# Performance work log

Hardware: AMD Instinct MI355X
Metric: run time of the kernel (lower is better)

## Reference

```python
import jax, jax.numpy as jnp
import numpy as np

N = 50000       # nodes
E = 800000      # edges
D = 128         # in_channels == hidden*heads
H = 8           # heads
C = 16          # hidden_channels (per-head dim)
L = 4           # num_layers
OUT = 128       # out_channels


def setup_inputs() -> dict:
    key = jax.random.key(0)
    ks = jax.random.split(key, 16)
    s = 1.0 / np.sqrt(D)
    inp = {
        "x": jax.random.normal(ks[0], (N, D), dtype=jnp.float32),
        "edge_index": jax.random.randint(ks[1], (2, E), 0, N, dtype=jnp.int32),
        "batch": jnp.zeros((N,), dtype=jnp.int32),
        # stacked per-layer params (all layers are D->H*C with D == H*C)
        "Wq": jax.random.normal(ks[2], (L, D, H * C), dtype=jnp.float32) * s,
        "bq": jnp.zeros((L, H * C), dtype=jnp.float32),
        "Wk": jax.random.normal(ks[3], (L, D, H * C), dtype=jnp.float32) * s,
        "bk": jnp.zeros((L, H * C), dtype=jnp.float32),
        "Wv": jax.random.normal(ks[4], (L, D, H * C), dtype=jnp.float32) * s,
        "bv": jnp.zeros((L, H * C), dtype=jnp.float32),
        "Wskip": jax.random.normal(ks[5], (L, D, H * C), dtype=jnp.float32) * s,
        "bskip": jnp.zeros((L, H * C), dtype=jnp.float32),
        "Wout": jax.random.normal(ks[6], (D, OUT), dtype=jnp.float32) * s,
        "bout": jnp.zeros((OUT,), dtype=jnp.float32),
    }
    return inp


def _transformer_conv(x, src, dst, Wq, bq, Wk, bk, Wv, bv, Wskip, bskip):
    # PyG TransformerConv (concat=True, root_weight=True, beta=False), eval mode
    q = (x @ Wq + bq).reshape(N, H, C)
    k = (x @ Wk + bk).reshape(N, H, C)
    v = (x @ Wv + bv).reshape(N, H, C)
    # edge-wise attention scores [E, H]
    score = jnp.einsum("ehc,ehc->eh", q[dst], k[src]) / jnp.sqrt(jnp.float32(C))
    # segment softmax over incoming edges of each dst node
    m = jax.ops.segment_max(score, dst, num_segments=N)          # [N, H]
    p = jnp.exp(score - m[dst])                                  # [E, H]
    z = jax.ops.segment_sum(p, dst, num_segments=N)              # [N, H]
    alpha = p / z[dst]                                           # [E, H]
    msg = alpha[:, :, None] * v[src]                             # [E, H, C]
    agg = jax.ops.segment_sum(msg, dst, num_segments=N)          # [N, H, C]
    return agg.reshape(N, H * C) + (x @ Wskip + bskip)


def reference(x, edge_index, batch, Wq, bq, Wk, bk, Wv, bv, Wskip, bskip, Wout, bout):
    src = edge_index[0]
    dst = edge_index[1]
    for l in range(L):
        x = _transformer_conv(x, src, dst, Wq[l], bq[l], Wk[l], bk[l],
                              Wv[l], bv[l], Wskip[l], bskip[l])
        x = jax.nn.relu(x)  # dropout is identity in eval mode
    return x @ Wout + bout
```

## Files before the change

kernel.cpp:

```cpp
#include <hip/hip_runtime.h>
#include <hip/hip_fp16.h>
#include <math.h>

#define NN 50000
#define EE 800000
#define DD 128

typedef __attribute__((ext_vector_type(8))) _Float16 half8;
typedef __attribute__((ext_vector_type(2))) _Float16 h2;
typedef __attribute__((ext_vector_type(4))) float f32x4;

#if __has_builtin(__builtin_amdgcn_fdot2)
#define FDOT2(a,b,c) __builtin_amdgcn_fdot2((a),(b),(c),false)
#else
static __device__ __forceinline__ float FDOT2(h2 a, h2 b, float c){
  return c + (float)a[0]*(float)b[0] + (float)a[1]*(float)b[1];
}
#endif


__global__ void zero_kernel(int* __restrict__ p, int n){
  int i = blockIdx.x*blockDim.x + threadIdx.x;
  if (i < n) p[i] = 0;
}

__global__ void hist_kernel(const int* __restrict__ edst, int* __restrict__ deg, int e){
  int i = blockIdx.x*blockDim.x + threadIdx.x;
  if (i < e) atomicAdd(&deg[edst[i]], 1);
}

__global__ void scan_partial(const int* __restrict__ deg, int* __restrict__ bsum, int n){
  __shared__ int s[256];
  int t = threadIdx.x;
  int i = blockIdx.x*256 + t;
  s[t] = (i < n) ? deg[i] : 0;
  __syncthreads();
  for (int o = 128; o > 0; o >>= 1){
    if (t < o) s[t] += s[t+o];
    __syncthreads();
  }
  if (t == 0) bsum[blockIdx.x] = s[0];
}

__global__ void scan_bsums(int* __restrict__ bsum, int nb){
  __shared__ int s[256];
  int t = threadIdx.x;
  int v = (t < nb) ? bsum[t] : 0;
  s[t] = v;
  __syncthreads();
  for (int o = 1; o < 256; o <<= 1){
    int x = (t >= o) ? s[t-o] : 0;
    __syncthreads();
    s[t] += x;
    __syncthreads();
  }
  if (t < nb) bsum[t] = s[t] - v;
}

__global__ void scan_apply(const int* __restrict__ deg, const int* __restrict__ bsum,
                           int* __restrict__ off, int* __restrict__ cursor, int n){
  __shared__ int s[256];
  int t = threadIdx.x;
  int i = blockIdx.x*256 + t;
  int v = (i < n) ? deg[i] : 0;
  s[t] = v;
  __syncthreads();
  for (int o = 1; o < 256; o <<= 1){
    int x = (t >= o) ? s[t-o] : 0;
    __syncthreads();
    s[t] += x;
    __syncthreads();
  }
  int excl = s[t] - v + bsum[blockIdx.x];
  if (i < n){
    off[i] = excl;
    if (i < n-1) cursor[i] = excl;
  }
}

__global__ void scatter_kernel(const int* __restrict__ esrc, const int* __restrict__ edst,
                               int* __restrict__ cursor, int* __restrict__ csr_src, int e){
  int i = blockIdx.x*blockDim.x + threadIdx.x;
  if (i < e){
    int d = edst[i];
    int pos = atomicAdd(&cursor[d], 1);
    csr_src[pos] = esrc[i];
  }
}

__global__ void prep_w(const float* __restrict__ Wq, const float* __restrict__ Wk,
                       const float* __restrict__ Wv, const float* __restrict__ Ws,
                       const float* __restrict__ bq, const float* __restrict__ bk,
                       const float* __restrict__ bv, const float* __restrict__ bs,
                       const float* __restrict__ Wout,
                       __half* __restrict__ wt, float* __restrict__ bcat,
                       __half* __restrict__ wtout){
  int idx = blockIdx.x*256 + threadIdx.x;
  if (idx < 4*512*128){
    int l = idx >> 16;
    int rem = idx & 65535;
    int n = rem >> 7;
    int k = rem & 127;
    int mat = n >> 7;
    int nn = n & 127;
    const float* W = (mat==0)?Wq:(mat==1)?Wk:(mat==2)?Wv:Ws;
    wt[idx] = __float2half(W[l*16384 + k*128 + nn]);
  }
  if (idx < 128*128){
    int n = idx >> 7, k = idx & 127;
    wtout[idx] = __float2half(Wout[k*128 + n]);
  }
  if (idx < 4*512){
    int l = idx >> 9, n = idx & 511;
    int mat = n >> 7, nn = n & 127;
    const float* B = (mat==0)?bq:(mat==1)?bk:(mat==2)?bv:bs;
    bcat[idx] = B[l*128 + nn];
  }
}

__global__ void convert_x(const float* __restrict__ x, __half* __restrict__ xh, int n8){
  int i = blockIdx.x*256 + threadIdx.x;
  if (i < n8){
    float4 f0 = *(const float4*)&x[(size_t)i*8];
    float4 f1 = *(const float4*)&x[(size_t)i*8+4];
    __half2 h[4] = {__floats2half2_rn(f0.x,f0.y), __floats2half2_rn(f0.z,f0.w),
                    __floats2half2_rn(f1.x,f1.y), __floats2half2_rn(f1.z,f1.w)};
    *(int4*)&xh[(size_t)i*8] = *(const int4*)h;
  }
}

template<int FMODE>
__global__ __launch_bounds__(256) void mfma_gemm(
    const __half* __restrict__ xh, const __half* __restrict__ wt,
    const float* __restrict__ bias,
    __half* __restrict__ oq, __half* __restrict__ okv, __half* __restrict__ osk,
    float* __restrict__ ofp, int nrows)
{
  __shared__ __half sh[32768];
  __half* a_lds = sh;
  __half* b_lds = sh + 16384;

  const int tid = threadIdx.x;
  const int m0 = blockIdx.x * 128;
  const int by = blockIdx.y;
  const int n0 = by * 128;

  #pragma unroll
  for (int p = 0; p < 8; p++){
    int chunk = tid + p*256;
    int row = chunk >> 4;
    int cs  = chunk & 15;
    int swz = cs ^ (row & 7);
    int gm = m0 + row;
    int4 va = make_int4(0,0,0,0);
    if (gm < nrows) va = *(const int4*)&xh[(size_t)gm*DD + cs*8];
    *(int4*)&a_lds[row*128 + swz*8] = va;
    int4 vb = *(const int4*)&wt[(size_t)(n0+row)*DD + cs*8];
    *(int4*)&b_lds[row*128 + swz*8] = vb;
  }
  __syncthreads();

  const int lane = tid & 63;
  const int w  = tid >> 6;
  const int wr = w >> 1, wc = w & 1;
  const int li = lane & 15, lg = lane >> 4;

  f32x4 acc[4][4];
  #pragma unroll
  for (int fn = 0; fn < 4; fn++){
    float b = bias[n0 + wc*64 + fn*16 + li];
    #pragma unroll
    for (int fm = 0; fm < 4; fm++)
      acc[fm][fn] = (f32x4){b, b, b, b};
  }

  #pragma unroll
  for (int kk = 0; kk < 4; kk++){
    half8 af[4], bf[4];
    #pragma unroll
    for (int fm = 0; fm < 4; fm++){
      int row = wr*64 + fm*16 + li;
      int chunk = kk*4 + lg;
      af[fm] = *(half8*)&a_lds[row*128 + (chunk ^ (row & 7))*8];
    }
    #pragma unroll
    for (int fn = 0; fn < 4; fn++){
      int row = wc*64 + fn*16 + li;
      int chunk = kk*4 + lg;
      bf[fn] = *(half8*)&b_lds[row*128 + (chunk ^ (row & 7))*8];
    }
    #pragma unroll
    for (int fm = 0; fm < 4; fm++)
      #pragma unroll
      for (int fn = 0; fn < 4; fn++)
        acc[fm][fn] = __builtin_amdgcn_mfma_f32_16x16x32_f16(af[fm], bf[fn], acc[fm][fn], 0, 0, 0);
  }

  if (FMODE == 0){
    __syncthreads();
    #pragma unroll
    for (int fm = 0; fm < 4; fm++)
      #pragma unroll
      for (int fn = 0; fn < 4; fn++)
        #pragma unroll
        for (int r = 0; r < 4; r++){
          int row = wr*64 + fm*16 + lg*4 + r;
          int col = wc*64 + fn*16 + li;
          int chunk = col >> 3, within = col & 7;
          a_lds[row*128 + (chunk ^ (row & 7))*8 + within] = __float2half(acc[fm][fn][r]);
        }
    __syncthreads();
    __half* dst;
    int ostride;
    if (by == 0)      { dst = oq;        ostride = 128; }
    else if (by == 1) { dst = okv;       ostride = 256; }
    else if (by == 2) { dst = okv + 128; ostride = 256; }
    else              { dst = osk;       ostride = 128; }
    #pragma unroll
    for (int p = 0; p < 8; p++){
      int chunk = tid + p*256;
      int row = chunk >> 4, cs = chunk & 15;
      int gm = m0 + row;
      if (gm < nrows)
        *(int4*)&dst[(size_t)gm*ostride + cs*8] = *(int4*)&a_lds[row*128 + (cs ^ (row & 7))*8];
    }
  } else {
    __syncthreads();
    float* f_lds = (float*)sh;
    #pragma unroll
    for (int fm = 0; fm < 4; fm++)
      #pragma unroll
      for (int fn = 0; fn < 4; fn++)
        #pragma unroll
        for (int r = 0; r < 4; r++){
          int row = wr*64 + fm*16 + lg*4 + r;
          int col = wc*64 + fn*16 + li;
          int chunk = col >> 2, within = col & 3;
          f_lds[row*128 + (chunk ^ (row & 7))*4 + within] = acc[fm][fn][r];
        }
    __syncthreads();
    #pragma unroll
    for (int p = 0; p < 16; p++){
      int chunk = tid + p*256;
      int row = chunk >> 5, cs = chunk & 31;
      int gm = m0 + row;
      if (gm < nrows)
        *(int4*)&ofp[(size_t)gm*DD + cs*4] = *(int4*)&f_lds[row*128 + (cs ^ (row & 7))*4];
    }
  }
}

__global__ __launch_bounds__(256) void agg_kernel(
    const __half* __restrict__ hq, const __half* __restrict__ hsk,
    const __half* __restrict__ kv,
    const int* __restrict__ off, const int* __restrict__ csr_src,
    __half* __restrict__ xout, int n)
{
  int wid = blockIdx.x*4 + (threadIdx.x >> 6);
  if (wid >= n) return;
  int lane = threadIdx.x & 63;
  int sub  = lane >> 3;
  int h    = lane & 7;
  int c    = h*16;

  int4 q0 = *(const int4*)&hq[(size_t)wid*DD + c];
  int4 q1 = *(const int4*)&hq[(size_t)wid*DD + c + 8];

  float z = 0.f;
  float acc[16];
  #pragma unroll
  for (int i = 0; i < 16; i++) acc[i] = 0.f;

  const int e1 = off[wid+1];
  int e = off[wid] + sub;
  int s2 = (e+8 < e1) ? csr_src[e+8] : -1;
  int4 k0r, k1r, v0r, v1r;
  if (e < e1){
    const __half* r = kv + (size_t)csr_src[e]*256 + c;
    k0r = *(const int4*)r;        k1r = *(const int4*)(r+8);
    v0r = *(const int4*)(r+128);  v1r = *(const int4*)(r+136);
  }
  while (e < e1){
    int4 k0n, k1n, v0n, v1n;
    if (s2 >= 0){
      const __half* r = kv + (size_t)s2*256 + c;
      k0n = *(const int4*)r;        k1n = *(const int4*)(r+8);
      v0n = *(const int4*)(r+128);  v1n = *(const int4*)(r+136);
    }
    int s3 = (e+16 < e1) ? csr_src[e+16] : -1;

    const h2* kh0 = (const h2*)&k0r;
    const h2* kh1 = (const h2*)&k1r;
    const h2* qh0 = (const h2*)&q0;
    const h2* qh1 = (const h2*)&q1;
    float p = 0.f;
    #pragma unroll
    for (int i = 0; i < 4; i++) p = FDOT2(kh0[i], qh0[i], p);
    #pragma unroll
    for (int i = 0; i < 4; i++) p = FDOT2(kh1[i], qh1[i], p);
    float wgt = __expf(p * 0.25f);

    const __half2* vh0 = (const __half2*)&v0r;
    const __half2* vh1 = (const __half2*)&v1r;
    #pragma unroll
    for (int i = 0; i < 4; i++){
      float2 f = __half22float2(vh0[i]);
      acc[2*i]   += wgt * f.x;
      acc[2*i+1] += wgt * f.y;
    }
    #pragma unroll
    for (int i = 0; i < 4; i++){
      float2 f = __half22float2(vh1[i]);
      acc[8+2*i]   += wgt * f.x;
      acc[8+2*i+1] += wgt * f.y;
    }
    z += wgt;

    k0r = k0n; k1r = k1n; v0r = v0n; v1r = v1n;
    s2 = s3; e += 8;
  }

  #pragma unroll
  for (int d = 8; d <= 32; d <<= 1){
    z += __shfl_xor(z, d);
    #pragma unroll
    for (int i = 0; i < 16; i++)
      acc[i] += __shfl_xor(acc[i], d);
  }

  if (sub == 0){
    float inv = (z > 0.f) ? 1.f/z : 0.f;
    int4 s0 = *(const int4*)&hsk[(size_t)wid*DD + c];
    int4 s1 = *(const int4*)&hsk[(size_t)wid*DD + c + 8];
    const __half2* sh0 = (const __half2*)&s0;
    const __half2* sh1 = (const __half2*)&s1;
    __half2 po[4];
    #pragma unroll
    for (int i = 0; i < 4; i++){
      float2 s = __half22float2(sh0[i]);
      po[i] = __floats2half2_rn(fmaxf(acc[2*i]*inv + s.x, 0.f),
                                fmaxf(acc[2*i+1]*inv + s.y, 0.f));
    }
    *(int4*)&xout[(size_t)wid*DD + c] = *(const int4*)po;
    #pragma unroll
    for (int i = 0; i < 4; i++){
      float2 s = __half22float2(sh1[i]);
      po[i] = __floats2half2_rn(fmaxf(acc[8+2*i]*inv + s.x, 0.f),
                                fmaxf(acc[8+2*i+1]*inv + s.y, 0.f));
    }
    *(int4*)&xout[(size_t)wid*DD + c + 8] = *(const int4*)po;
  }
}


extern "C" void kernel_launch(void* const* d_in, const int* in_sizes, int n_in,
                              void* d_out, int out_size, void* d_ws, size_t ws_size,
                              hipStream_t stream) {
  const float* x     = (const float*)d_in[0];
  const int*   edge  = (const int*)d_in[1];
  const int*   esrc  = edge;
  const int*   edst  = edge + EE;
  const float* Wq    = (const float*)d_in[3];
  const float* bq    = (const float*)d_in[4];
  const float* Wk    = (const float*)d_in[5];
  const float* bk    = (const float*)d_in[6];
  const float* Wv    = (const float*)d_in[7];
  const float* bv    = (const float*)d_in[8];
  const float* Wsk   = (const float*)d_in[9];
  const float* bsk   = (const float*)d_in[10];
  const float* Wout  = (const float*)d_in[11];
  const float* bout  = (const float*)d_in[12];
  float* out = (float*)d_out;

  uintptr_t base = (uintptr_t)d_ws;
  auto align = [](uintptr_t p){ return (p + 255) & ~(uintptr_t)255; };
  int* deg    = (int*)base;  base = align(base + (NN+1)*sizeof(int));
  int* off    = (int*)base;  base = align(base + (NN+1)*sizeof(int));
  int* cursor = (int*)base;  base = align(base + NN*sizeof(int));
  int* bsum   = (int*)base;  base = align(base + 256*sizeof(int));
  int* csr    = (int*)base;  base = align(base + (size_t)EE*sizeof(int));
  __half* xh   = (__half*)base; base = align(base + (size_t)NN*DD*sizeof(__half));
  __half* xbuf = (__half*)base; base = align(base + (size_t)NN*DD*sizeof(__half));
  __half* hq   = (__half*)base; base = align(base + (size_t)NN*DD*sizeof(__half));
  __half* hsk  = (__half*)base; base = align(base + (size_t)NN*DD*sizeof(__half));
  __half* kvb  = (__half*)base; base = align(base + (size_t)NN*256*sizeof(__half));
  __half* wt   = (__half*)base; base = align(base + (size_t)4*512*128*sizeof(__half));
  __half* wtout= (__half*)base; base = align(base + (size_t)128*128*sizeof(__half));
  float*  bcat = (float*)base;  base = align(base + (size_t)4*512*sizeof(float));

  const int NP = NN + 1;
  const int SCAN_BLKS = (NP + 255)/256;

  zero_kernel<<<SCAN_BLKS, 256, 0, stream>>>(deg, NP);
  hist_kernel<<<(EE+255)/256, 256, 0, stream>>>(edst, deg, EE);
  scan_partial<<<SCAN_BLKS, 256, 0, stream>>>(deg, bsum, NP);
  scan_bsums<<<1, 256, 0, stream>>>(bsum, SCAN_BLKS);
  scan_apply<<<SCAN_BLKS, 256, 0, stream>>>(deg, bsum, off, cursor, NP);
  scatter_kernel<<<(EE+255)/256, 256, 0, stream>>>(esrc, edst, cursor, csr, EE);

  prep_w<<<1024, 256, 0, stream>>>(Wq, Wk, Wv, Wsk, bq, bk, bv, bsk, Wout, wt, bcat, wtout);
  convert_x<<<(NN*DD/8 + 255)/256, 256, 0, stream>>>(x, xh, NN*DD/8);

  const int MT = (NN + 127)/128;
  const __half* xin = xh;
  for (int l = 0; l < 4; l++){
    mfma_gemm<0><<<dim3(MT, 4), 256, 0, stream>>>(
        xin, wt + (size_t)l*512*128, bcat + l*512,
        hq, kvb, hsk, nullptr, NN);
    agg_kernel<<<(NN+3)/4, 256, 0, stream>>>(hq, hsk, kvb, off, csr, xbuf, NN);
    xin = xbuf;
  }
  mfma_gemm<1><<<dim3(MT, 1), 256, 0, stream>>>(
      xin, wtout, bout, nullptr, nullptr, nullptr, out, NN);
}
```

Measured before the change: 455.0 us.

## Store Q and KV head-major and split aggregation per head

The GEMM epilogue now writes Q and the interleaved K/V rows in head-major order ([H][N][16] and [H][N][32]), so each head's data forms a compact 3.2 MB (Q) or 6.4 MB (KV) slab. The aggregation kernel assigns one block per (16-node chunk, head), with 16 lanes per node striding over edges. The aim is better cache locality for random source gathers within a head. The trade-offs are that the software prefetch of the next edge is removed, the CSR index array is read eight times (once per head), and the GEMM stores become scattered 16-byte writes.

```diff
diff --git a/kernel.cpp b/kernel.cpp
--- a/kernel.cpp
+++ b/kernel.cpp
@@ -210,19 +210,24 @@
           a_lds[row*128 + (chunk ^ (row & 7))*8 + within] = __float2half(acc[fm][fn][r]);
         }
     __syncthreads();
-    __half* dst;
-    int ostride;
-    if (by == 0)      { dst = oq;        ostride = 128; }
-    else if (by == 1) { dst = okv;       ostride = 256; }
-    else if (by == 2) { dst = okv + 128; ostride = 256; }
-    else              { dst = osk;       ostride = 128; }
     #pragma unroll
     for (int p = 0; p < 8; p++){
       int chunk = tid + p*256;
       int row = chunk >> 4, cs = chunk & 15;
       int gm = m0 + row;
-      if (gm < nrows)
-        *(int4*)&dst[(size_t)gm*ostride + cs*8] = *(int4*)&a_lds[row*128 + (cs ^ (row & 7))*8];
+      if (gm >= nrows) continue;
+      int4 val = *(int4*)&a_lds[row*128 + (cs ^ (row & 7))*8];
+      if (by == 3){
+        *(int4*)&osk[(size_t)gm*DD + cs*8] = val;
+      } else {
+        int h = cs >> 1;
+        int ho = (cs & 1)*8;
+        __half* dst;
+        if (by == 0)      dst = oq  + ((size_t)h*NN + gm)*16 + ho;
+        else if (by == 1) dst = okv + ((size_t)h*NN + gm)*32 + ho;
+        else              dst = okv + ((size_t)h*NN + gm)*32 + 16 + ho;
+        *(int4*)dst = val;
+      }
     }
   } else {
     __syncthreads();
@@ -251,48 +256,41 @@
 }
 
 __global__ __launch_bounds__(256) void agg_kernel(
-    const __half* __restrict__ hq, const __half* __restrict__ hsk,
-    const __half* __restrict__ kv,
+    const __half* __restrict__ qh, const __half* __restrict__ hsk,
+    const __half* __restrict__ kvh,
     const int* __restrict__ off, const int* __restrict__ csr_src,
     __half* __restrict__ xout, int n)
 {
-  int wid = blockIdx.x*4 + (threadIdx.x >> 6);
-  if (wid >= n) return;
-  int lane = threadIdx.x & 63;
-  int sub  = lane >> 3;
-  int h    = lane & 7;
-  int c    = h*16;
-
-  int4 q0 = *(const int4*)&hq[(size_t)wid*DD + c];
-  int4 q1 = *(const int4*)&hq[(size_t)wid*DD + c + 8];
+  const int h     = blockIdx.x & 7;
+  const int chunk = blockIdx.x >> 3;
+  const int tid = threadIdx.x;
+  const int g   = tid >> 4;
+  const int l   = tid & 15;
+  const int nd  = chunk*16 + g;
+  if (nd >= n) return;
+
+  const __half* qp = qh + ((size_t)h*NN + nd)*16;
+  int4 q0 = *(const int4*)qp;
+  int4 q1 = *(const int4*)(qp + 8);
+  const h2* qh0 = (const h2*)&q0;
+  const h2* qh1 = (const h2*)&q1;
 
   float z = 0.f;
   float acc[16];
   #pragma unroll
   for (int i = 0; i < 16; i++) acc[i] = 0.f;
 
-  const int e1 = off[wid+1];
-  int e = off[wid] + sub;
-  int s2 = (e+8 < e1) ? csr_src[e+8] : -1;
-  int4 k0r, k1r, v0r, v1r;
-  if (e < e1){
-    const __half* r = kv + (size_t)csr_src[e]*256 + c;
-    k0r = *(const int4*)r;        k1r = *(const int4*)(r+8);
-    v0r = *(const int4*)(r+128);  v1r = *(const int4*)(r+136);
-  }
-  while (e < e1){
-    int4 k0n, k1n, v0n, v1n;
-    if (s2 >= 0){
-      const __half* r = kv + (size_t)s2*256 + c;
-      k0n = *(const int4*)r;        k1n = *(const int4*)(r+8);
-      v0n = *(const int4*)(r+128);  v1n = *(const int4*)(r+136);
-    }
-    int s3 = (e+16 < e1) ? csr_src[e+16] : -1;
-
-    const h2* kh0 = (const h2*)&k0r;
-    const h2* kh1 = (const h2*)&k1r;
-    const h2* qh0 = (const h2*)&q0;
-    const h2* qh1 = (const h2*)&q1;
+  const int e1 = off[nd+1];
+  for (int e = off[nd] + l; e < e1; e += 16){
+    int s = csr_src[e];
+    const __half* r = kvh + ((size_t)h*NN + s)*32;
+    int4 k0 = *(const int4*)r;
+    int4 k1 = *(const int4*)(r + 8);
+    int4 v0 = *(const int4*)(r + 16);
+    int4 v1 = *(const int4*)(r + 24);
+
+    const h2* kh0 = (const h2*)&k0;
+    const h2* kh1 = (const h2*)&k1;
     float p = 0.f;
     #pragma unroll
     for (int i = 0; i < 4; i++) p = FDOT2(kh0[i], qh0[i], p);
@@ -300,8 +298,8 @@
     for (int i = 0; i < 4; i++) p = FDOT2(kh1[i], qh1[i], p);
     float wgt = __expf(p * 0.25f);
 
-    const __half2* vh0 = (const __half2*)&v0r;
-    const __half2* vh1 = (const __half2*)&v1r;
+    const __half2* vh0 = (const __half2*)&v0;
+    const __half2* vh1 = (const __half2*)&v1;
     #pragma unroll
     for (int i = 0; i < 4; i++){
       float2 f = __half22float2(vh0[i]);
@@ -315,23 +313,21 @@
       acc[8+2*i+1] += wgt * f.y;
     }
     z += wgt;
-
-    k0r = k0n; k1r = k1n; v0r = v0n; v1r = v1n;
-    s2 = s3; e += 8;
   }
 
   #pragma unroll
-  for (int d = 8; d <= 32; d <<= 1){
+  for (int d = 1; d <= 8; d <<= 1){
     z += __shfl_xor(z, d);
     #pragma unroll
     for (int i = 0; i < 16; i++)
       acc[i] += __shfl_xor(acc[i], d);
   }
 
-  if (sub == 0){
+  if (l == 0){
     float inv = (z > 0.f) ? 1.f/z : 0.f;
-    int4 s0 = *(const int4*)&hsk[(size_t)wid*DD + c];
-    int4 s1 = *(const int4*)&hsk[(size_t)wid*DD + c + 8];
+    const __half* sp = hsk + (size_t)nd*DD + h*16;
+    int4 s0 = *(const int4*)sp;
+    int4 s1 = *(const int4*)(sp + 8);
     const __half2* sh0 = (const __half2*)&s0;
     const __half2* sh1 = (const __half2*)&s1;
     __half2 po[4];
@@ -341,14 +337,14 @@
       po[i] = __floats2half2_rn(fmaxf(acc[2*i]*inv + s.x, 0.f),
                                 fmaxf(acc[2*i+1]*inv + s.y, 0.f));
     }
-    *(int4*)&xout[(size_t)wid*DD + c] = *(const int4*)po;
+    *(int4*)&xout[(size_t)nd*DD + h*16] = *(const int4*)po;
     #pragma unroll
     for (int i = 0; i < 4; i++){
       float2 s = __half22float2(sh1[i]);
       po[i] = __floats2half2_rn(fmaxf(acc[8+2*i]*inv + s.x, 0.f),
                                 fmaxf(acc[8+2*i+1]*inv + s.y, 0.f));
     }
-    *(int4*)&xout[(size_t)wid*DD + c + 8] = *(const int4*)po;
+    *(int4*)&xout[(size_t)nd*DD + h*16 + 8] = *(const int4*)po;
   }
 }
 
@@ -381,9 +377,9 @@
   int* csr    = (int*)base;  base = align(base + (size_t)EE*sizeof(int));
   __half* xh   = (__half*)base; base = align(base + (size_t)NN*DD*sizeof(__half));
   __half* xbuf = (__half*)base; base = align(base + (size_t)NN*DD*sizeof(__half));
-  __half* hq   = (__half*)base; base = align(base + (size_t)NN*DD*sizeof(__half));
+  __half* qhd  = (__half*)base; base = align(base + (size_t)NN*DD*sizeof(__half));
   __half* hsk  = (__half*)base; base = align(base + (size_t)NN*DD*sizeof(__half));
-  __half* kvb  = (__half*)base; base = align(base + (size_t)NN*256*sizeof(__half));
+  __half* kvh  = (__half*)base; base = align(base + (size_t)NN*256*sizeof(__half));
   __half* wt   = (__half*)base; base = align(base + (size_t)4*512*128*sizeof(__half));
   __half* wtout= (__half*)base; base = align(base + (size_t)128*128*sizeof(__half));
   float*  bcat = (float*)base;  base = align(base + (size_t)4*512*sizeof(float));
@@ -402,12 +398,13 @@
   convert_x<<<(NN*DD/8 + 255)/256, 256, 0, stream>>>(x, xh, NN*DD/8);
 
   const int MT = (NN + 127)/128;
+  const int AGG_BLKS = ((NN + 15)/16) * 8;
   const __half* xin = xh;
   for (int l = 0; l < 4; l++){
     mfma_gemm<0><<<dim3(MT, 4), 256, 0, stream>>>(
         xin, wt + (size_t)l*512*128, bcat + l*512,
-        hq, kvb, hsk, nullptr, NN);
-    agg_kernel<<<(NN+3)/4, 256, 0, stream>>>(hq, hsk, kvb, off, csr, xbuf, NN);
+        qhd, kvh, hsk, nullptr, NN);
+    agg_kernel<<<AGG_BLKS, 256, 0, stream>>>(qhd, hsk, kvh, off, csr, xbuf, NN);
     xin = xbuf;
   }
   mfma_gemm<1><<<dim3(MT, 1), 256, 0, stream>>>(
```

Result: slower. 545.8 us (+20.0%).

## Reuse A tile across all four weight matrices in one GEMM block

Applied to the files above, without the earlier changes.

The GEMM now uses 64-row tiles and loops over the four projection matrices inside a single block. Each A tile is loaded from global memory once instead of four times, and the 2D grid becomes 1D. The B tile is reloaded serially for each matrix, with extra syncs and no overlap between loads and compute. That adds serial latency per block, and the smaller tile halves MFMA work per block.

```diff
diff --git a/kernel.cpp b/kernel.cpp
--- a/kernel.cpp
+++ b/kernel.cpp
@@ -136,116 +136,120 @@
     __half* __restrict__ oq, __half* __restrict__ okv, __half* __restrict__ osk,
     float* __restrict__ ofp, int nrows)
 {
-  __shared__ __half sh[32768];
-  __half* a_lds = sh;
-  __half* b_lds = sh + 16384;
+  __shared__ __half a_lds[64*128];
+  __shared__ __half b_lds[128*128];
 
   const int tid = threadIdx.x;
-  const int m0 = blockIdx.x * 128;
-  const int by = blockIdx.y;
-  const int n0 = by * 128;
-
-  #pragma unroll
-  for (int p = 0; p < 8; p++){
-    int chunk = tid + p*256;
-    int row = chunk >> 4;
-    int cs  = chunk & 15;
-    int swz = cs ^ (row & 7);
-    int gm = m0 + row;
-    int4 va = make_int4(0,0,0,0);
-    if (gm < nrows) va = *(const int4*)&xh[(size_t)gm*DD + cs*8];
-    *(int4*)&a_lds[row*128 + swz*8] = va;
-    int4 vb = *(const int4*)&wt[(size_t)(n0+row)*DD + cs*8];
-    *(int4*)&b_lds[row*128 + swz*8] = vb;
-  }
-  __syncthreads();
-
+  const int m0 = blockIdx.x * 64;
   const int lane = tid & 63;
   const int w  = tid >> 6;
   const int wr = w >> 1, wc = w & 1;
   const int li = lane & 15, lg = lane >> 4;
 
-  f32x4 acc[4][4];
   #pragma unroll
-  for (int fn = 0; fn < 4; fn++){
-    float b = bias[n0 + wc*64 + fn*16 + li];
-    #pragma unroll
-    for (int fm = 0; fm < 4; fm++)
-      acc[fm][fn] = (f32x4){b, b, b, b};
-  }
-
-  #pragma unroll
-  for (int kk = 0; kk < 4; kk++){
-    half8 af[4], bf[4];
-    #pragma unroll
-    for (int fm = 0; fm < 4; fm++){
-      int row = wr*64 + fm*16 + li;
-      int chunk = kk*4 + lg;
-      af[fm] = *(half8*)&a_lds[row*128 + (chunk ^ (row & 7))*8];
-    }
-    #pragma unroll
-    for (int fn = 0; fn < 4; fn++){
-      int row = wc*64 + fn*16 + li;
-      int chunk = kk*4 + lg;
-      bf[fn] = *(half8*)&b_lds[row*128 + (chunk ^ (row & 7))*8];
-    }
-    #pragma unroll
-    for (int fm = 0; fm < 4; fm++)
-      #pragma unroll
-      for (int fn = 0; fn < 4; fn++)
-        acc[fm][fn] = __builtin_amdgcn_mfma_f32_16x16x32_f16(af[fm], bf[fn], acc[fm][fn], 0, 0, 0);
-  }
-
-  if (FMODE == 0){
-    __syncthreads();
-    #pragma unroll
-    for (int fm = 0; fm < 4; fm++)
-      #pragma unroll
-      for (int fn = 0; fn < 4; fn++)
-        #pragma unroll
-        for (int r = 0; r < 4; r++){
-          int row = wr*64 + fm*16 + lg*4 + r;
-          int col = wc*64 + fn*16 + li;
-          int chunk = col >> 3, within = col & 7;
-          a_lds[row*128 + (chunk ^ (row & 7))*8 + within] = __float2half(acc[fm][fn][r]);
-        }
-    __syncthreads();
-    __half* dst;
-    int ostride;
-    if (by == 0)      { dst = oq;        ostride = 128; }
-    else if (by == 1) { dst = okv;       ostride = 256; }
-    else if (by == 2) { dst = okv + 128; ostride = 256; }
-    else              { dst = osk;       ostride = 128; }
+  for (int p = 0; p < 4; p++){
+    int chunk = tid + p*256;
+    int row = chunk >> 4;
+    int cs  = chunk & 15;
+    int gm = m0 + row;
+    int4 va = make_int4(0,0,0,0);
+    if (gm < nrows) va = *(const int4*)&xh[(size_t)gm*DD + cs*8];
+    *(int4*)&a_lds[row*128 + (cs ^ (row & 7))*8] = va;
+  }
+
+  const int NMATS = (FMODE == 0) ? 4 : 1;
+  for (int mat = 0; mat < NMATS; mat++){
     #pragma unroll
     for (int p = 0; p < 8; p++){
       int chunk = tid + p*256;
-      int row = chunk >> 4, cs = chunk & 15;
-      int gm = m0 + row;
-      if (gm < nrows)
-        *(int4*)&dst[(size_t)gm*ostride + cs*8] = *(int4*)&a_lds[row*128 + (cs ^ (row & 7))*8];
-    }
-  } else {
-    __syncthreads();
-    float* f_lds = (float*)sh;
-    #pragma unroll
-    for (int fm = 0; fm < 4; fm++)
-      #pragma unroll
-      for (int fn = 0; fn < 4; fn++)
+      int row = chunk >> 4;
+      int cs  = chunk & 15;
+      int4 vb = *(const int4*)&wt[(size_t)(mat*128 + row)*DD + cs*8];
+      *(int4*)&b_lds[row*128 + (cs ^ (row & 7))*8] = vb;
+    }
+    __syncthreads();
+
+    f32x4 acc[2][4];
+    #pragma unroll
+    for (int fn = 0; fn < 4; fn++){
+      float b = bias[mat*128 + wc*64 + fn*16 + li];
+      #pragma unroll
+      for (int fm = 0; fm < 2; fm++)
+        acc[fm][fn] = (f32x4){b, b, b, b};
+    }
+
+    #pragma unroll
+    for (int kk = 0; kk < 4; kk++){
+      half8 af[2], bf[4];
+      #pragma unroll
+      for (int fm = 0; fm < 2; fm++){
+        int row = wr*32 + fm*16 + li;
+        int chunk = kk*4 + lg;
+        af[fm] = *(half8*)&a_lds[row*128 + (chunk ^ (row & 7))*8];
+      }
+      #pragma unroll
+      for (int fn = 0; fn < 4; fn++){
+        int row = wc*64 + fn*16 + li;
+        int chunk = kk*4 + lg;
+        bf[fn] = *(half8*)&b_lds[row*128 + (chunk ^ (row & 7))*8];
+      }
+      #pragma unroll
+      for (int fm = 0; fm < 2; fm++)
         #pragma unroll
-        for (int r = 0; r < 4; r++){
-          int row = wr*64 + fm*16 + lg*4 + r;
-          int col = wc*64 + fn*16 + li;
-          int chunk = col >> 2, within = col & 3;
-          f_lds[row*128 + (chunk ^ (row & 7))*4 + within] = acc[fm][fn][r];
+        for (int fn = 0; fn < 4; fn++)
+          acc[fm][fn] = __builtin_amdgcn_mfma_f32_16x16x32_f16(af[fm], bf[fn], acc[fm][fn], 0, 0, 0);
+    }
+    __syncthreads();
+
+    if (FMODE == 0){
+      #pragma unroll
+      for (int fm = 0; fm < 2; fm++)
+        #pragma unroll
+        for (int fn = 0; fn < 4; fn++)
+          #pragma unroll
+          for (int r = 0; r < 4; r++){
+            int row = wr*32 + fm*16 + lg*4 + r;
+            int col = wc*64 + fn*16 + li;
+            int chunk = col >> 3, within = col & 7;
+            b_lds[row*128 + (chunk ^ (row & 7))*8 + within] = __float2half(acc[fm][fn][r]);
+          }
+      __syncthreads();
+      #pragma unroll
+      for (int p = 0; p < 4; p++){
+        int chunk = tid + p*256;
+        int row = chunk >> 4, cs = chunk & 15;
+        int gm = m0 + row;
+        if (gm < nrows){
+          int4 val = *(int4*)&b_lds[row*128 + (cs ^ (row & 7))*8];
+          if (mat == 0)      *(int4*)&oq [(size_t)gm*128 + cs*8]       = val;
+          else if (mat == 1) *(int4*)&okv[(size_t)gm*256 + cs*8]       = val;
+          else if (mat == 2) *(int4*)&okv[(size_t)gm*256 + 128 + cs*8] = val;
+          else               *(int4*)&osk[(size_t)gm*128 + cs*8]       = val;
         }
-    __syncthreads();
-    #pragma unroll
-    for (int p = 0; p < 16; p++){
-      int chunk = tid + p*256;
-      int row = chunk >> 5, cs = chunk & 31;
-      int gm = m0 + row;
-      if (gm < nrows)
-        *(int4*)&ofp[(size_t)gm*DD + cs*4] = *(int4*)&f_lds[row*128 + (cs ^ (row & 7))*4];
+      }
+      __syncthreads();
+    } else {
+      float* f_lds = (float*)b_lds;
+      #pragma unroll
+      for (int fm = 0; fm < 2; fm++)
+        #pragma unroll
+        for (int fn = 0; fn < 4; fn++)
+          #pragma unroll
+          for (int r = 0; r < 4; r++){
+            int row = wr*32 + fm*16 + lg*4 + r;
+            int col = wc*64 + fn*16 + li;
+            int chunk = col >> 2, within = col & 3;
+            f_lds[row*128 + (chunk ^ (row & 7))*4 + within] = acc[fm][fn][r];
+          }
+      __syncthreads();
+      #pragma unroll
+      for (int p = 0; p < 8; p++){
+        int chunk = tid + p*256;
+        int row = chunk >> 5, cs = chunk & 31;
+        int gm = m0 + row;
+        if (gm < nrows)
+          *(int4*)&ofp[(size_t)gm*DD + cs*4] = *(int4*)&f_lds[row*128 + (cs ^ (row & 7))*4];
+      }
     }
   }
 }
@@ -265,6 +269,8 @@
 
   int4 q0 = *(const int4*)&hq[(size_t)wid*DD + c];
   int4 q1 = *(const int4*)&hq[(size_t)wid*DD + c + 8];
+  const h2* qh0 = (const h2*)&q0;
+  const h2* qh1 = (const h2*)&q1;
 
   float z = 0.f;
   float acc[16];
@@ -291,8 +297,6 @@
 
     const h2* kh0 = (const h2*)&k0r;
     const h2* kh1 = (const h2*)&k1r;
-    const h2* qh0 = (const h2*)&q0;
-    const h2* qh1 = (const h2*)&q1;
     float p = 0.f;
     #pragma unroll
     for (int i = 0; i < 4; i++) p = FDOT2(kh0[i], qh0[i], p);
@@ -401,15 +405,15 @@
   prep_w<<<1024, 256, 0, stream>>>(Wq, Wk, Wv, Wsk, bq, bk, bv, bsk, Wout, wt, bcat, wtout);
   convert_x<<<(NN*DD/8 + 255)/256, 256, 0, stream>>>(x, xh, NN*DD/8);
 
-  const int MT = (NN + 127)/128;
+  const int MT64 = (NN + 63)/64;
   const __half* xin = xh;
   for (int l = 0; l < 4; l++){
-    mfma_gemm<0><<<dim3(MT, 4), 256, 0, stream>>>(
+    mfma_gemm<0><<<MT64, 256, 0, stream>>>(
         xin, wt + (size_t)l*512*128, bcat + l*512,
         hq, kvb, hsk, nullptr, NN);
     agg_kernel<<<(NN+3)/4, 256, 0, stream>>>(hq, hsk, kvb, off, csr, xbuf, NN);
     xin = xbuf;
   }
-  mfma_gemm<1><<<dim3(MT, 1), 256, 0, stream>>>(
+  mfma_gemm<1><<<MT64, 256, 0, stream>>>(
       xin, wtout, bout, nullptr, nullptr, nullptr, out, NN);
 }
```

Result: faster. 437.3 us (-3.9%).
